# Optimization experiments

Hardware: AMD Instinct MI355X
Metric: run time of the kernel (lower is better)

## Reference

```python
import jax, jax.numpy as jnp
import numpy as np

N_VERTICES = 1_000_000
N_DIM = 128
B = 16384
K = 10

def setup_inputs() -> dict:
    key = jax.random.key(0)
    k1, k2, k3, k4, k5 = jax.random.split(key, 5)
    emb_table = jax.random.normal(k1, (N_VERTICES, N_DIM), dtype=jnp.float32) * 0.01
    pos_v = jax.random.randint(k2, (B,), 0, N_VERTICES)
    pos_u = jax.random.randint(k3, (B,), 0, N_VERTICES)
    neg_v = jax.random.randint(k4, (B, K), 0, N_VERTICES)
    weights = jax.random.uniform(k5, (B,), dtype=jnp.float32)
    return {"pos_v": pos_v, "pos_u": pos_u, "neg_v": neg_v,
            "weights": weights, "emb_table": emb_table}

def reference(pos_v, pos_u, neg_v, weights, emb_table):
    emb_v = emb_table[pos_v]            # [B, d]
    emb_u = emb_table[pos_u]            # [B, d]
    emb_neg_v = emb_table[neg_v]        # [B, K, d]
    # batched dot: [B,K,d] x [B,d] -> [B,K]
    neg_score = jnp.einsum('bkd,bd->bk', emb_neg_v, emb_v)
    neg_score = jax.nn.log_sigmoid(-neg_score).sum(axis=1)   # [B]
    pos_score = jnp.sum(emb_v * emb_u, axis=1)               # [B]
    score = jax.nn.log_sigmoid(pos_score) + neg_score
    return -jnp.sum(weights * score)
```

## Files before the change

### kernel.cpp

```cpp
#include <hip/hip_runtime.h>
#include <math.h>
#include <stdint.h>

constexpr int BATCH = 16384;
constexpr int KNEG  = 10;
constexpr int DIM   = 128;
constexpr int SLOTS_PER_ITEM = 12;
constexpr int NPAIR = BATCH * SLOTS_PER_ITEM;
constexpr int NBUCKET = 2048;
constexpr int BUCKET_SHIFT = 9;

constexpr int ITEMS_PER_BLOCK = 8;
constexpr int NBLK_COMPUTE = BATCH / ITEMS_PER_BLOCK;
constexpr int PAIRS_PER_BLOCK = 32;
constexpr int NBLK_GATHER = NPAIR / PAIRS_PER_BLOCK;

constexpr size_t WS_CNT   = 0;
constexpr size_t WS_CUR   = 16384;
constexpr size_t WS_PAIRS = 32768;
constexpr size_t WS_D     = 2097152;
constexpr size_t WS_PART  = 102760448;

__device__ __forceinline__ float log_sigmoid(float x) {
    return fminf(x, 0.0f) - log1pf(expf(-fabsf(x)));
}

__device__ __forceinline__ int slot_row(int slot,
                                        const int* __restrict__ pos_v,
                                        const int* __restrict__ pos_u,
                                        const int* __restrict__ neg_v) {
    int item = slot / SLOTS_PER_ITEM;
    int j    = slot - item * SLOTS_PER_ITEM;
    if (j < KNEG) return neg_v[item * KNEG + j];
    return (j == KNEG) ? pos_v[item] : pos_u[item];
}

__global__ void k0_zero(unsigned int* __restrict__ cnt) {
    int t = blockIdx.x * blockDim.x + threadIdx.x;
    if (t < NBUCKET) cnt[t] = 0u;
}

__global__ __launch_bounds__(256) void k1_count(
    const int* __restrict__ pos_v, const int* __restrict__ pos_u,
    const int* __restrict__ neg_v, unsigned int* __restrict__ cnt) {
    int slot = blockIdx.x * blockDim.x + threadIdx.x;
    int row  = slot_row(slot, pos_v, pos_u, neg_v);
    atomicAdd(&cnt[row >> BUCKET_SHIFT], 1u);
}

__global__ __launch_bounds__(256) void k2_scan(
    const unsigned int* __restrict__ cnt, unsigned int* __restrict__ cur) {
    int t = threadIdx.x;
    unsigned int local[8];
    unsigned int s = 0;
#pragma unroll
    for (int i = 0; i < 8; ++i) { local[i] = cnt[t * 8 + i]; s += local[i]; }

    unsigned int v = s;
#pragma unroll
    for (int d = 1; d < 64; d <<= 1) {
        unsigned int n = __shfl_up(v, d, 64);
        if ((t & 63) >= d) v += n;
    }
    __shared__ unsigned int wsum[4];
    if ((t & 63) == 63) wsum[t >> 6] = v;
    __syncthreads();
    unsigned int woff = 0;
    for (int w = 0; w < (t >> 6); ++w) woff += wsum[w];
    unsigned int run = woff + v - s;
#pragma unroll
    for (int i = 0; i < 8; ++i) { cur[t * 8 + i] = run; run += local[i]; }
}

__global__ __launch_bounds__(256) void k3_scatter(
    const int* __restrict__ pos_v, const int* __restrict__ pos_u,
    const int* __restrict__ neg_v, unsigned int* __restrict__ cur,
    uint64_t* __restrict__ pairs) {
    int slot = blockIdx.x * blockDim.x + threadIdx.x;
    int row  = slot_row(slot, pos_v, pos_u, neg_v);
    unsigned int p = atomicAdd(&cur[row >> BUCKET_SHIFT], 1u);
    pairs[p] = ((uint64_t)(unsigned int)row << 32) | (unsigned int)slot;
}

__global__ __launch_bounds__(256) void k4_gather(
    const uint64_t* __restrict__ pairs, const float* __restrict__ emb,
    float* __restrict__ D) {
    int bid = blockIdx.x;
    constexpr int q = NBLK_GATHER / 8;
    int swz = (bid % 8) * q + bid / 8;
    int lane = threadIdx.x & 31;
    int grp  = threadIdx.x >> 5;
    int base = swz * PAIRS_PER_BLOCK;

    float4 r[4];
    uint32_t slot[4];
#pragma unroll
    for (int i = 0; i < 4; ++i) {
        uint64_t p = pairs[base + grp + i * 8];
        slot[i] = (uint32_t)p;
        const float4* src = (const float4*)(emb + (size_t)(p >> 32) * DIM);
        r[i] = src[lane];
    }
#pragma unroll
    for (int i = 0; i < 4; ++i) {
        float4* dst = (float4*)(D + (size_t)slot[i] * DIM);
        dst[lane] = r[i];
    }
}

__global__ __launch_bounds__(256, 4) void k5_compute(
    const float* __restrict__ D, const float* __restrict__ weights,
    float* __restrict__ partials) {
    const int tid  = threadIdx.x;
    const int lane = tid & 31;
    const int item = tid >> 5;
    const int b    = blockIdx.x * ITEMS_PER_BLOCK + item;
    const size_t sbase = (size_t)b * SLOTS_PER_ITEM * DIM;

    const float4* vrow = (const float4*)(D + sbase + (size_t)KNEG * DIM);
    const float4* urow = (const float4*)(D + sbase + (size_t)(KNEG + 1) * DIM);
    const float4 v = vrow[lane];
    const float4 u = urow[lane];

    float dots[KNEG + 1];
    dots[KNEG] = v.x * u.x + v.y * u.y + v.z * u.z + v.w * u.w;
#pragma unroll
    for (int k = 0; k < KNEG; ++k) {
        const float4 n = ((const float4*)(D + sbase + (size_t)k * DIM))[lane];
        dots[k] = v.x * n.x + v.y * n.y + v.z * n.z + v.w * n.w;
    }
#pragma unroll
    for (int k = 0; k <= KNEG; ++k) {
#pragma unroll
        for (int off = 16; off; off >>= 1)
            dots[k] += __shfl_down(dots[k], off, 32);
    }

    __shared__ float partial[ITEMS_PER_BLOCK];
    if (lane == 0) {
        float s = log_sigmoid(dots[KNEG]);
#pragma unroll
        for (int k = 0; k < KNEG; ++k)
            s += log_sigmoid(-dots[k]);
        partial[item] = weights[b] * s;
    }
    __syncthreads();
    if (tid == 0) {
        float acc = 0.0f;
#pragma unroll
        for (int i = 0; i < ITEMS_PER_BLOCK; ++i) acc += partial[i];
        partials[blockIdx.x] = acc;
    }
}

__global__ __launch_bounds__(256) void k6_reduce(
    const float* __restrict__ partials, float* __restrict__ out) {
    const int tid = threadIdx.x;
    float acc = 0.0f;
#pragma unroll
    for (int i = 0; i < NBLK_COMPUTE / 256; ++i)
        acc += partials[tid + i * 256];
#pragma unroll
    for (int off = 32; off; off >>= 1)
        acc += __shfl_down(acc, off, 64);
    __shared__ float sp[4];
    if ((tid & 63) == 0) sp[tid >> 6] = acc;
    __syncthreads();
    if (tid == 0)
        out[0] = -(sp[0] + sp[1] + sp[2] + sp[3]);
}

extern "C" void kernel_launch(void* const* d_in, const int* in_sizes, int n_in,
                              void* d_out, int out_size, void* d_ws, size_t ws_size,
                              hipStream_t stream) {
    const int*   pos_v   = (const int*)d_in[0];
    const int*   pos_u   = (const int*)d_in[1];
    const int*   neg_v   = (const int*)d_in[2];
    const float* weights = (const float*)d_in[3];
    const float* emb     = (const float*)d_in[4];
    float*       out     = (float*)d_out;
    char*        ws      = (char*)d_ws;

    unsigned int* cnt   = (unsigned int*)(ws + WS_CNT);
    unsigned int* cur   = (unsigned int*)(ws + WS_CUR);
    uint64_t*     pairs = (uint64_t*)(ws + WS_PAIRS);
    float*        D     = (float*)(ws + WS_D);
    float*        part  = (float*)(ws + WS_PART);

    k0_zero   <<<dim3((NBUCKET + 255) / 256), 256, 0, stream>>>(cnt);
    k1_count  <<<dim3(NPAIR / 256), 256, 0, stream>>>(pos_v, pos_u, neg_v, cnt);
    k2_scan   <<<dim3(1), 256, 0, stream>>>(cnt, cur);
    k3_scatter<<<dim3(NPAIR / 256), 256, 0, stream>>>(pos_v, pos_u, neg_v, cur, pairs);
    k4_gather <<<dim3(NBLK_GATHER), 256, 0, stream>>>(pairs, emb, D);
    k5_compute<<<dim3(NBLK_COMPUTE), 256, 0, stream>>>(D, weights, part);
    k6_reduce <<<dim3(1), 256, 0, stream>>>(part, out);
}
```

Measured before the change: 669.0 us.

## Replace random row gather with per-bucket sequential streaming of embedding rows

The gather kernel now runs one block per 512-row bucket. Each block builds a shared-memory histogram and counting sort of the requested rows in its bucket, then streams every table row in the bucket sequentially, with a one-row register prefetch. Each loaded row is written to all slots that request it, so random row reads become contiguous reads. The cost is reading the whole table, about five times the bytes actually needed, with only a shallow per-group prefetch. Buckets holding more than 384 pairs fall back to a direct gather.

```diff
diff --git a/kernel.cpp b/kernel.cpp
--- a/kernel.cpp
+++ b/kernel.cpp
@@ -2,6 +2,7 @@
 #include <math.h>
 #include <stdint.h>
 
+constexpr int N_VERT = 1000000;
 constexpr int BATCH = 16384;
 constexpr int KNEG  = 10;
 constexpr int DIM   = 128;
@@ -9,11 +10,11 @@
 constexpr int NPAIR = BATCH * SLOTS_PER_ITEM;
 constexpr int NBUCKET = 2048;
 constexpr int BUCKET_SHIFT = 9;
+constexpr int ROWS_PER_BUCKET = 512;
+constexpr int CAP = 384;
 
 constexpr int ITEMS_PER_BLOCK = 8;
 constexpr int NBLK_COMPUTE = BATCH / ITEMS_PER_BLOCK;
-constexpr int PAIRS_PER_BLOCK = 32;
-constexpr int NBLK_GATHER = NPAIR / PAIRS_PER_BLOCK;
 
 constexpr size_t WS_CNT   = 0;
 constexpr size_t WS_CUR   = 16384;
@@ -82,29 +83,92 @@
     pairs[p] = ((uint64_t)(unsigned int)row << 32) | (unsigned int)slot;
 }
 
-__global__ __launch_bounds__(256) void k4_gather(
+__global__ __launch_bounds__(256, 4) void k4_stream(
+    const unsigned int* __restrict__ cnt, const unsigned int* __restrict__ cur,
     const uint64_t* __restrict__ pairs, const float* __restrict__ emb,
     float* __restrict__ D) {
-    int bid = blockIdx.x;
-    constexpr int q = NBLK_GATHER / 8;
-    int swz = (bid % 8) * q + bid / 8;
-    int lane = threadIdx.x & 31;
-    int grp  = threadIdx.x >> 5;
-    int base = swz * PAIRS_PER_BLOCK;
-
-    float4 r[4];
-    uint32_t slot[4];
-#pragma unroll
-    for (int i = 0; i < 4; ++i) {
-        uint64_t p = pairs[base + grp + i * 8];
-        slot[i] = (uint32_t)p;
-        const float4* src = (const float4*)(emb + (size_t)(p >> 32) * DIM);
-        r[i] = src[lane];
-    }
-#pragma unroll
-    for (int i = 0; i < 4; ++i) {
-        float4* dst = (float4*)(D + (size_t)slot[i] * DIM);
-        dst[lane] = r[i];
+    const int b    = blockIdx.x;
+    const int tid  = threadIdx.x;
+    const int lane = tid & 31;
+    const int grp  = tid >> 5;
+    const int row0 = b * ROWS_PER_BUCKET;
+
+    const unsigned int n     = cnt[b];
+    const unsigned int start = cur[b] - n;
+    if (n == 0) return;
+
+    __shared__ unsigned int hcnt[ROWS_PER_BUCKET + 1];
+    __shared__ unsigned int hstart[ROWS_PER_BUCKET + 1];
+    __shared__ unsigned int hcur[ROWS_PER_BUCKET];
+    __shared__ unsigned int tsorted[CAP];
+    __shared__ unsigned int wsum[4];
+
+    if (n <= CAP) {
+        for (int i = tid; i < ROWS_PER_BUCKET + 1; i += 256) hcnt[i] = 0u;
+        __syncthreads();
+        for (unsigned int i = tid; i < n; i += 256) {
+            unsigned int rl = (unsigned int)(pairs[start + i] >> 32) - row0;
+            atomicAdd(&hcnt[rl], 1u);
+        }
+        __syncthreads();
+        {
+            unsigned int a  = hcnt[2 * tid];
+            unsigned int b2 = hcnt[2 * tid + 1];
+            unsigned int s  = a + b2;
+            unsigned int v  = s;
+#pragma unroll
+            for (int d = 1; d < 64; d <<= 1) {
+                unsigned int nn = __shfl_up(v, d, 64);
+                if ((tid & 63) >= d) v += nn;
+            }
+            if ((tid & 63) == 63) wsum[tid >> 6] = v;
+            __syncthreads();
+            unsigned int woff = 0;
+            for (int w = 0; w < (tid >> 6); ++w) woff += wsum[w];
+            unsigned int ex = woff + v - s;
+            hstart[2 * tid]     = ex;
+            hstart[2 * tid + 1] = ex + a;
+            hcur[2 * tid]       = ex;
+            hcur[2 * tid + 1]   = ex + a;
+            if (tid == 255) hstart[ROWS_PER_BUCKET] = woff + v;
+        }
+        __syncthreads();
+        for (unsigned int i = tid; i < n; i += 256) {
+            uint64_t p  = pairs[start + i];
+            unsigned int rl   = (unsigned int)(p >> 32) - row0;
+            unsigned int pos  = atomicAdd(&hcur[rl], 1u);
+            tsorted[pos] = (rl << 18) | (unsigned int)p;
+        }
+        __syncthreads();
+
+        int rl = grp;
+        int row = row0 + rl;
+        float4 curreg = make_float4(0.f, 0.f, 0.f, 0.f);
+        if (row < N_VERT)
+            curreg = ((const float4*)(emb + (size_t)row * DIM))[lane];
+        for (int t = 0; t < ROWS_PER_BUCKET / 8; ++t) {
+            float4 nxt = make_float4(0.f, 0.f, 0.f, 0.f);
+            int rln = rl + 8;
+            if (t + 1 < ROWS_PER_BUCKET / 8 && row0 + rln < N_VERT)
+                nxt = ((const float4*)(emb + (size_t)(row0 + rln) * DIM))[lane];
+            if (row0 + rl < N_VERT) {
+                unsigned int s = hstart[rl], e = hstart[rl + 1];
+                for (unsigned int j = s; j < e; ++j) {
+                    unsigned int slot = tsorted[j] & 0x3FFFFu;
+                    ((float4*)(D + (size_t)slot * DIM))[lane] = curreg;
+                }
+            }
+            curreg = nxt;
+            rl = rln;
+        }
+    } else {
+        for (unsigned int i = grp; i < n; i += 8) {
+            uint64_t p = pairs[start + i];
+            unsigned int row  = (unsigned int)(p >> 32);
+            unsigned int slot = (unsigned int)p;
+            float4 r = ((const float4*)(emb + (size_t)row * DIM))[lane];
+            ((float4*)(D + (size_t)slot * DIM))[lane] = r;
+        }
     }
 }
 
@@ -191,7 +255,7 @@
     k1_count  <<<dim3(NPAIR / 256), 256, 0, stream>>>(pos_v, pos_u, neg_v, cnt);
     k2_scan   <<<dim3(1), 256, 0, stream>>>(cnt, cur);
     k3_scatter<<<dim3(NPAIR / 256), 256, 0, stream>>>(pos_v, pos_u, neg_v, cur, pairs);
-    k4_gather <<<dim3(NBLK_GATHER), 256, 0, stream>>>(pairs, emb, D);
+    k4_stream <<<dim3(NBUCKET), 256, 0, stream>>>(cnt, cur, pairs, emb, D);
     k5_compute<<<dim3(NBLK_COMPUTE), 256, 0, stream>>>(D, weights, part);
     k6_reduce <<<dim3(1), 256, 0, stream>>>(part, out);
 }
```

Result: slower. 760.6 us (+13.7%).
